# Kernel optimization log

Measured on AMD Instinct MI355X. Metric: run time of the kernel, lower is better.

Reference implementation:

```python
import jax, jax.numpy as jnp
import numpy as np

RESO = 32          # grid_resolution
HID = 32           # hidden_dim
CDIM = 32          # c_dim
NBLK = 5           # n_blocks
PAD = 0.1          # padding
L = 10             # positional encoding frequencies -> dim 60


def setup_inputs() -> dict:
    key = jax.random.key(0)
    ks = jax.random.split(key, 12)
    B, T = 2, 200000
    p = jax.random.uniform(ks[0], (B, T, 3), jnp.float32, -0.5, 0.5)
    s = 0.05
    return {
        "p": p,
        "fc_pos_w": jax.random.normal(ks[1], (60, 2 * HID), jnp.float32) * s,
        "fc_pos_b": jax.random.normal(ks[2], (2 * HID,), jnp.float32) * s,
        "blk_fc0_w": jax.random.normal(ks[3], (NBLK, 2 * HID, HID), jnp.float32) * s,
        "blk_fc0_b": jax.random.normal(ks[4], (NBLK, HID), jnp.float32) * s,
        "blk_fc1_w": jax.random.normal(ks[5], (NBLK, HID, HID), jnp.float32) * s,
        "blk_fc1_b": jax.random.normal(ks[6], (NBLK, HID), jnp.float32) * s,
        "blk_sc_w": jax.random.normal(ks[7], (NBLK, 2 * HID, HID), jnp.float32) * s,  # shortcut, no bias
        "fc_c_w": jax.random.normal(ks[8], (HID, CDIM), jnp.float32) * s,
        "fc_c_b": jax.random.normal(ks[9], (CDIM,), jnp.float32) * s,
    }


def _pos_encode(p):
    # p in [-0.5,0.5] -> [-2,0] after 2p-1 (matches torch impl: p = 2*p - 1)
    q = 2.0 * p - 1.0
    freqs = (jnp.pi * (2.0 ** jnp.arange(L, dtype=jnp.float32)))  # [L]
    a = q[..., None, :] * freqs[:, None]                          # [B,T,L,3]
    pe = jnp.stack([jnp.sin(a), jnp.cos(a)], axis=-2)             # [B,T,L,2,3]
    return pe.reshape(*p.shape[:-1], 2 * L * 3)                   # [B,T,60]


def _normalize_3d(p):
    p_nor = p / (1.0 + PAD + 1e-3) + 0.5
    return jnp.clip(p_nor, 0.0, 1.0 - 1e-3)


def _coord2index(p_nor):
    x = jnp.floor(p_nor * RESO).astype(jnp.int32)                  # [B,T,3]
    return x[..., 0] + RESO * (x[..., 1] + RESO * x[..., 2])       # [B,T]


def _resblock(x, w0, b0, w1, b1, ws):
    h = jax.nn.relu(jax.nn.relu(x) @ w0 + b0)
    return x @ ws + (jax.nn.relu(h) @ w1 + b1)


def reference(p, fc_pos_w, fc_pos_b, blk_fc0_w, blk_fc0_b, blk_fc1_w, blk_fc1_b,
              blk_sc_w, fc_c_w, fc_c_b):
    B, T, _ = p.shape
    G = RESO ** 3
    p_nor = _normalize_3d(p)
    idx = _coord2index(p_nor)                                      # [B,T]
    gidx = (idx + jnp.arange(B, dtype=jnp.int32)[:, None] * G).reshape(-1)  # [B*T]

    net = _pos_encode(p) @ fc_pos_w + fc_pos_b                     # [B,T,64]
    net = _resblock(net, blk_fc0_w[0], blk_fc0_b[0], blk_fc1_w[0], blk_fc1_b[0], blk_sc_w[0])
    for i in range(1, NBLK):
        # pool_local: scatter_max per grid cell, gather back to points
        flat = net.reshape(B * T, HID)
        cell = jax.ops.segment_max(flat, gidx, num_segments=B * G)  # [B*G,HID]
        pooled = cell[gidx].reshape(B, T, HID)
        net = jnp.concatenate([net, pooled], axis=-1)               # [B,T,64]
        net = _resblock(net, blk_fc0_w[i], blk_fc0_b[i], blk_fc1_w[i], blk_fc1_b[i], blk_sc_w[i])

    c = net @ fc_c_w + fc_c_b                                       # [B,T,CDIM]

    # generate_grid_features: scatter_mean into grid (empty cells = 0)
    cf = c.reshape(B * T, CDIM)
    sums = jax.ops.segment_sum(cf, gidx, num_segments=B * G)        # [B*G,CDIM]
    cnt = jax.ops.segment_sum(jnp.ones((B * T, 1), c.dtype), gidx, num_segments=B * G)
    mean = sums / jnp.maximum(cnt, 1.0)
    fea_grid = mean.reshape(B, G, CDIM).transpose(0, 2, 1).reshape(B, CDIM, RESO, RESO, RESO)
    return fea_grid
```

## Files before the change

kernel.cpp:

```cpp
#include <hip/hip_runtime.h>
#include <math.h>

#define TPTS 200000
#define BB 2
#define NPTS (BB*TPTS)
#define GRID3 32768
#define BG 65536
#define SROWS 176

typedef __attribute__((ext_vector_type(8))) __bf16 bf16x8;
typedef __attribute__((ext_vector_type(4))) float f32x4;
typedef unsigned short ushort_t;

#define MFMA16(a,b,c) __builtin_amdgcn_mfma_f32_16x16x32_bf16(a,b,c,0,0,0)

__device__ __forceinline__ void split8(const float* v, bf16x8& hi, bf16x8& lo)
{
#pragma unroll
  for (int j = 0; j < 8; j++) {
    float f = v[j];
    __bf16 h = (__bf16)f;
    hi[j] = h;
    lo[j] = (__bf16)(f - (float)h);
  }
}

__device__ __forceinline__ void relumask8(
    const float* v, const bf16x8& xh, const bf16x8& xl, bf16x8& rh, bf16x8& rl)
{
#pragma unroll
  for (int j = 0; j < 8; j++) {
    bool neg = v[j] < 0.f;
    rh[j] = neg ? (__bf16)0.f : xh[j];
    rl[j] = neg ? (__bf16)0.f : xl[j];
  }
}

__device__ __forceinline__ int cellof(float p0, float p1, float p2, int t)
{
  const float DEN = (float)(1.0 + 0.1 + 1e-3);
  const float HI  = (float)(1.0 - 1e-3);
  float n0 = fminf(fmaxf(p0/DEN + 0.5f, 0.f), HI);
  float n1 = fminf(fmaxf(p1/DEN + 0.5f, 0.f), HI);
  float n2 = fminf(fmaxf(p2/DEN + 0.5f, 0.f), HI);
  int c0 = (int)floorf(n0*32.f), c1 = (int)floorf(n1*32.f), c2 = (int)floorf(n2*32.f);
  return c0 + 32*(c1 + 32*c2) + (t >= TPTS ? GRID3 : 0);
}

__global__ __launch_bounds__(256) void k_hist(
    const float* __restrict__ p, int* __restrict__ gbuf, int* __restrict__ hist)
{
  int t = blockIdx.x*256 + threadIdx.x;
  if (t >= NPTS) return;
  int g = cellof(p[3*t], p[3*t+1], p[3*t+2], t);
  gbuf[t] = g;
  atomicAdd(hist + g, 1);
}

__global__ __launch_bounds__(256) void k_scanA(
    const int* __restrict__ hist, int* __restrict__ texcl, int* __restrict__ bsum)
{
  __shared__ int sm[256];
  int tid = threadIdx.x;
  int t = blockIdx.x*256 + tid;
  int v = hist[t];
  sm[tid] = v; __syncthreads();
  for (int off = 1; off < 256; off <<= 1) {
    int x = sm[tid];
    int u = (tid >= off) ? sm[tid-off] : 0;
    __syncthreads();
    sm[tid] = x + u;
    __syncthreads();
  }
  texcl[t] = sm[tid] - v;
  if (tid == 255) bsum[blockIdx.x] = sm[255];
}

__global__ __launch_bounds__(256) void k_scanB(
    const int* __restrict__ bsum, int* __restrict__ boff)
{
  __shared__ int sm[256];
  int tid = threadIdx.x;
  int v = bsum[tid];
  sm[tid] = v; __syncthreads();
  for (int off = 1; off < 256; off <<= 1) {
    int x = sm[tid];
    int u = (tid >= off) ? sm[tid-off] : 0;
    __syncthreads();
    sm[tid] = x + u;
    __syncthreads();
  }
  boff[tid] = sm[tid] - v;
}

__global__ __launch_bounds__(256) void k_scanC(
    const int* __restrict__ texcl, const int* __restrict__ boff,
    int* __restrict__ start, int* __restrict__ cursor)
{
  int t = blockIdx.x*256 + threadIdx.x;
  int v = boff[blockIdx.x] + texcl[t];
  start[t] = v; cursor[t] = v;
  if (t == 0) start[BG] = NPTS;
}

__global__ __launch_bounds__(256) void k_scatter(
    const float* __restrict__ p, const int* __restrict__ gbuf,
    int* __restrict__ cursor, float* __restrict__ p_sorted, int* __restrict__ gsort)
{
  int t = blockIdx.x*256 + threadIdx.x;
  if (t >= NPTS) return;
  int g = gbuf[t];
  int slot = atomicAdd(cursor + g, 1);
  gsort[slot] = g;
  p_sorted[3*slot]   = p[3*t];
  p_sorted[3*slot+1] = p[3*t+1];
  p_sorted[3*slot+2] = p[3*t+2];
}

__global__ void k_pack(
    const float* __restrict__ f0w, const float* __restrict__ scw,
    const float* __restrict__ f1w, const float* __restrict__ wc,
    const float* __restrict__ Wp,
    ushort_t* __restrict__ wpack)
{
  int f = blockIdx.x, l = threadIdx.x;
  if (f >= 104) {
    int idx = f - 104;
    int c = idx >> 3, t = (idx >> 1) & 3, e = idx & 1;
#pragma unroll
    for (int j = 0; j < 8; j++) {
      int k = c*32 + (l>>4)*8 + j, n = t*16 + (l&15);
      float v = (k < 60) ? Wp[k*64 + n] : 0.f;
      __bf16 h = (__bf16)v;
      __bf16 out = (e == 0) ? h : (__bf16)(v - (float)h);
      union { __bf16 b; ushort_t u; } cv; cv.b = out;
      wpack[((size_t)f*64 + l)*8 + j] = cv.u;
    }
    return;
  }
  const float* W; int c, t, e;
  if (f < 100) {
    int s = f / 20, r = f % 20;
    if (r < 8)       { W = f0w + s*2048; c = r>>2;        t = (r>>1)&1; e = r&1; }
    else if (r < 16) { int q = r-8;  W = scw + s*2048; c = q>>2; t = (q>>1)&1; e = q&1; }
    else             { int q = r-16; W = f1w + s*1024; c = 0;    t = q>>1;     e = q&1; }
  } else { int q = f-100; W = wc; c = 0; t = q>>1; e = q&1; }
#pragma unroll
  for (int j = 0; j < 8; j++) {
    int k = c*32 + (l>>4)*8 + j, n = t*16 + (l&15);
    float v = W[k*32 + n];
    __bf16 h = (__bf16)v;
    __bf16 out = (e == 0) ? h : (__bf16)(v - (float)h);
    union { __bf16 b; ushort_t u; } cv; cv.b = out;
    wpack[((size_t)f*64 + l)*8 + j] = cv.u;
  }
}

__global__ __launch_bounds__(256) void k_fused0(
    const float* __restrict__ ps,
    const ushort_t* __restrict__ wpPE, const float* __restrict__ bp,
    const ushort_t* __restrict__ wp,
    const float* __restrict__ b0, const float* __restrict__ b1,
    float* __restrict__ net)
{
  __shared__ float xlds[4][16*68];
  __shared__ float hbuf[4][16*36];
  int wave = threadIdx.x >> 6, lane = threadIdx.x & 63;
  int m = lane & 15, q = lane >> 4;
  int pbase = (blockIdx.x*4 + wave)*16;
  int pt = pbase + m;

  float p0 = ps[3*pt], p1 = ps[3*pt+1], p2 = ps[3*pt+2];
  float u0 = 2.f*p0 - 1.f, u1 = 2.f*p1 - 1.f, u2 = 2.f*p2 - 1.f;
  const float PIF = 3.14159265358979323846f;

  float pe[2][8];
#pragma unroll
  for (int c2 = 0; c2 < 2; c2++) {
#pragma unroll
    for (int jj = 0; jj < 8; jj++) {
      int e = c2*32 + q*8 + jj;
      int l = (e * 43691) >> 18;
      int r = e - l*6;
      bool issin = (r < 3);
      int d = issin ? r : (r - 3);
      float ud = (d == 0) ? u0 : ((d == 1) ? u1 : u2);
      float xval = ldexpf(ud, l);
      float red = xval - 2.f*rintf(0.5f*xval);
      float ang = PIF*red + (issin ? 0.f : 1.5707963267948966f);
      float v = __sinf(ang);
      pe[c2][jj] = (e < 60) ? v : 0.f;
    }
  }
  bf16x8 peh[2], pel[2];
  split8(pe[0], peh[0], pel[0]);
  split8(pe[1], peh[1], pel[1]);

  f32x4 xacc[4];
#pragma unroll
  for (int t = 0; t < 4; t++) {
    float bb = bp[t*16 + m];
    xacc[t] = (f32x4){bb,bb,bb,bb};
  }
#pragma unroll
  for (int c2 = 0; c2 < 2; c2++)
#pragma unroll
    for (int t = 0; t < 4; t++) {
      bf16x8 bh = *(const bf16x8*)(wpPE + ((size_t)((c2*4+t)*2    )*64 + lane)*8);
      bf16x8 bl = *(const bf16x8*)(wpPE + ((size_t)((c2*4+t)*2 + 1)*64 + lane)*8);
      xacc[t] = MFMA16(peh[c2], bh, xacc[t]);
      xacc[t] = MFMA16(pel[c2], bh, xacc[t]);
      xacc[t] = MFMA16(peh[c2], bl, xacc[t]);
    }

  float* xl = xlds[wave];
#pragma unroll
  for (int t = 0; t < 4; t++)
#pragma unroll
    for (int r = 0; r < 4; r++)
      xl[(q*4+r)*68 + t*16 + m] = xacc[t][r];
  __syncthreads();

  float xv[2][8];
#pragma unroll
  for (int c2 = 0; c2 < 2; c2++)
#pragma unroll
    for (int jj = 0; jj < 8; jj++)
      xv[c2][jj] = xl[m*68 + c2*32 + q*8 + jj];

  bf16x8 w0f[2][2][2], wsf[2][2][2], w1f[2][2];
#pragma unroll
  for (int c = 0; c < 2; c++)
#pragma unroll
    for (int t = 0; t < 2; t++)
#pragma unroll
      for (int e = 0; e < 2; e++) {
        w0f[c][t][e] = *(const bf16x8*)(wp + ((size_t)(((c*2+t)*2+e)    )*64 + lane)*8);
        wsf[c][t][e] = *(const bf16x8*)(wp + ((size_t)(((c*2+t)*2+e) + 8)*64 + lane)*8);
      }
#pragma unroll
  for (int t = 0; t < 2; t++)
#pragma unroll
    for (int e = 0; e < 2; e++)
      w1f[t][e] = *(const bf16x8*)(wp + ((size_t)(16 + t*2 + e)*64 + lane)*8);

  bf16x8 axh[2], axl[2], arh[2], arl[2];
#pragma unroll
  for (int c = 0; c < 2; c++) {
    split8(xv[c], axh[c], axl[c]);
    relumask8(xv[c], axh[c], axl[c], arh[c], arl[c]);
  }

  f32x4 hacc[2], yacc[2];
#pragma unroll
  for (int t = 0; t < 2; t++) {
    float bb0 = b0[m + 16*t], bb1 = b1[m + 16*t];
    hacc[t] = (f32x4){bb0,bb0,bb0,bb0};
    yacc[t] = (f32x4){bb1,bb1,bb1,bb1};
  }

#pragma unroll
  for (int c = 0; c < 2; c++)
#pragma unroll
    for (int t = 0; t < 2; t++) {
      hacc[t] = MFMA16(arh[c], w0f[c][t][0], hacc[t]);
      hacc[t] = MFMA16(arl[c], w0f[c][t][0], hacc[t]);
      hacc[t] = MFMA16(arh[c], w0f[c][t][1], hacc[t]);
      yacc[t] = MFMA16(axh[c], wsf[c][t][0], yacc[t]);
      yacc[t] = MFMA16(axl[c], wsf[c][t][0], yacc[t]);
      yacc[t] = MFMA16(axh[c], wsf[c][t][1], yacc[t]);
    }

  float* hb = hbuf[wave];
#pragma unroll
  for (int t = 0; t < 2; t++)
#pragma unroll
    for (int r = 0; r < 4; r++)
      hb[(q*4+r)*36 + m + 16*t] = fmaxf(hacc[t][r], 0.f);
  __syncthreads();
  float hv[8];
#pragma unroll
  for (int j = 0; j < 8; j++) hv[j] = hb[m*36 + q*8 + j];
  bf16x8 hh, hl; split8(hv, hh, hl);
#pragma unroll
  for (int t = 0; t < 2; t++) {
    yacc[t] = MFMA16(hh, w1f[t][0], yacc[t]);
    yacc[t] = MFMA16(hl, w1f[t][0], yacc[t]);
    yacc[t] = MFMA16(hh, w1f[t][1], yacc[t]);
  }

#pragma unroll
  for (int t = 0; t < 2; t++)
#pragma unroll
    for (int r = 0; r < 4; r++)
      net[(size_t)(pbase + q*4 + r)*32 + m + 16*t] = yacc[t][r];
}

__global__ __launch_bounds__(256) void k_stage_f(
    const float* __restrict__ netin, float* __restrict__ netout,
    const int* __restrict__ gsort, const int* __restrict__ start,
    const ushort_t* __restrict__ wp,
    const float* __restrict__ b0, const float* __restrict__ b1)
{
  __shared__ float sbuf[SROWS*36];
  int tid = threadIdx.x;
  int P0 = blockIdx.x*64;
  int s = start[gsort[P0]];
  int e = start[gsort[P0+63] + 1];
  int n = e - s; if (n > SROWS) n = SROWS;

  for (int idx = tid; idx < n*8; idx += 256) {
    int r = idx >> 3, c = idx & 7;
    *(f32x4*)(sbuf + r*36 + c*4) =
      *(const f32x4*)(netin + ((size_t)(s + r))*32 + c*4);
  }
  __syncthreads();

  int wave = tid >> 6, lane = tid & 63;
  int m = lane & 15, q = lane >> 4;
  int pbase = P0 + wave*16;
  int pt = pbase + m;
  int g = gsort[pt];
  int cs = start[g] - s, ce = start[g+1] - s;

  float xv[2][8];
  {
    const float* xr = sbuf + (pt - s)*36 + q*8;
    *(f32x4*)&xv[0][0] = *(const f32x4*)xr;
    *(f32x4*)&xv[0][4] = *(const f32x4*)(xr + 4);
  }
  {
    f32x4 ma = (f32x4){-INFINITY,-INFINITY,-INFINITY,-INFINITY};
    f32x4 mb = ma;
    for (int k = cs; k < ce; k++) {
      const float* rr = sbuf + k*36 + q*8;
      f32x4 va = *(const f32x4*)rr;
      f32x4 vb = *(const f32x4*)(rr + 4);
      ma.x = fmaxf(ma.x, va.x); ma.y = fmaxf(ma.y, va.y);
      ma.z = fmaxf(ma.z, va.z); ma.w = fmaxf(ma.w, va.w);
      mb.x = fmaxf(mb.x, vb.x); mb.y = fmaxf(mb.y, vb.y);
      mb.z = fmaxf(mb.z, vb.z); mb.w = fmaxf(mb.w, vb.w);
    }
    *(f32x4*)&xv[1][0] = ma;
    *(f32x4*)&xv[1][4] = mb;
  }

  bf16x8 w0f[2][2][2], wsf[2][2][2], w1f[2][2];
#pragma unroll
  for (int c = 0; c < 2; c++)
#pragma unroll
    for (int t = 0; t < 2; t++)
#pragma unroll
      for (int e2 = 0; e2 < 2; e2++) {
        w0f[c][t][e2] = *(const bf16x8*)(wp + ((size_t)(((c*2+t)*2+e2)    )*64 + lane)*8);
        wsf[c][t][e2] = *(const bf16x8*)(wp + ((size_t)(((c*2+t)*2+e2) + 8)*64 + lane)*8);
      }
#pragma unroll
  for (int t = 0; t < 2; t++)
#pragma unroll
    for (int e2 = 0; e2 < 2; e2++)
      w1f[t][e2] = *(const bf16x8*)(wp + ((size_t)(16 + t*2 + e2)*64 + lane)*8);

  bf16x8 axh[2], axl[2], arh[2], arl[2];
#pragma unroll
  for (int c = 0; c < 2; c++) {
    split8(xv[c], axh[c], axl[c]);
    relumask8(xv[c], axh[c], axl[c], arh[c], arl[c]);
  }

  f32x4 hacc[2], yacc[2];
#pragma unroll
  for (int t = 0; t < 2; t++) {
    float bb0 = b0[m + 16*t], bb1 = b1[m + 16*t];
    hacc[t] = (f32x4){bb0,bb0,bb0,bb0};
    yacc[t] = (f32x4){bb1,bb1,bb1,bb1};
  }

#pragma unroll
  for (int c = 0; c < 2; c++)
#pragma unroll
    for (int t = 0; t < 2; t++) {
      hacc[t] = MFMA16(arh[c], w0f[c][t][0], hacc[t]);
      hacc[t] = MFMA16(arl[c], w0f[c][t][0], hacc[t]);
      hacc[t] = MFMA16(arh[c], w0f[c][t][1], hacc[t]);
      yacc[t] = MFMA16(axh[c], wsf[c][t][0], yacc[t]);
      yacc[t] = MFMA16(axl[c], wsf[c][t][0], yacc[t]);
      yacc[t] = MFMA16(axh[c], wsf[c][t][1], yacc[t]);
    }

  __syncthreads();
  float* hb = sbuf + wave*576;
#pragma unroll
  for (int t = 0; t < 2; t++)
#pragma unroll
    for (int r = 0; r < 4; r++)
      hb[(q*4+r)*36 + m + 16*t] = fmaxf(hacc[t][r], 0.f);
  __syncthreads();
  float hv[8];
#pragma unroll
  for (int j = 0; j < 8; j++) hv[j] = hb[m*36 + q*8 + j];
  bf16x8 hh, hl; split8(hv, hh, hl);
#pragma unroll
  for (int t = 0; t < 2; t++) {
    yacc[t] = MFMA16(hh, w1f[t][0], yacc[t]);
    yacc[t] = MFMA16(hl, w1f[t][0], yacc[t]);
    yacc[t] = MFMA16(hh, w1f[t][1], yacc[t]);
  }

#pragma unroll
  for (int t = 0; t < 2; t++)
#pragma unroll
    for (int r = 0; r < 4; r++)
      netout[(size_t)(pbase + q*4 + r)*32 + m + 16*t] = yacc[t][r];
}

__global__ __launch_bounds__(256) void k_final_f(
    const float* __restrict__ netin, float* __restrict__ netout,
    const int* __restrict__ gsort, const int* __restrict__ start,
    const ushort_t* __restrict__ wp, const ushort_t* __restrict__ wpc,
    const float* __restrict__ b0, const float* __restrict__ b1,
    const float* __restrict__ bc)
{
  __shared__ float sbuf[SROWS*36];
  int tid = threadIdx.x;
  int P0 = blockIdx.x*64;
  int s = start[gsort[P0]];
  int e = start[gsort[P0+63] + 1];
  int n = e - s; if (n > SROWS) n = SROWS;

  for (int idx = tid; idx < n*8; idx += 256) {
    int r = idx >> 3, c = idx & 7;
    *(f32x4*)(sbuf + r*36 + c*4) =
      *(const f32x4*)(netin + ((size_t)(s + r))*32 + c*4);
  }
  __syncthreads();

  int wave = tid >> 6, lane = tid & 63;
  int m = lane & 15, q = lane >> 4;
  int pbase = P0 + wave*16;
  int pt = pbase + m;
  int g = gsort[pt];
  int cs = start[g] - s, ce = start[g+1] - s;

  float xv[2][8];
  {
    const float* xr = sbuf + (pt - s)*36 + q*8;
    *(f32x4*)&xv[0][0] = *(const f32x4*)xr;
    *(f32x4*)&xv[0][4] = *(const f32x4*)(xr + 4);
  }
  {
    f32x4 ma = (f32x4){-INFINITY,-INFINITY,-INFINITY,-INFINITY};
    f32x4 mb = ma;
    for (int k = cs; k < ce; k++) {
      const float* rr = sbuf + k*36 + q*8;
      f32x4 va = *(const f32x4*)rr;
      f32x4 vb = *(const f32x4*)(rr + 4);
      ma.x = fmaxf(ma.x, va.x); ma.y = fmaxf(ma.y, va.y);
      ma.z = fmaxf(ma.z, va.z); ma.w = fmaxf(ma.w, va.w);
      mb.x = fmaxf(mb.x, vb.x); mb.y = fmaxf(mb.y, vb.y);
      mb.z = fmaxf(mb.z, vb.z); mb.w = fmaxf(mb.w, vb.w);
    }
    *(f32x4*)&xv[1][0] = ma;
    *(f32x4*)&xv[1][4] = mb;
  }

  bf16x8 w0f[2][2][2], wsf[2][2][2], w1f[2][2], wcf[2][2];
#pragma unroll
  for (int c = 0; c < 2; c++)
#pragma unroll
    for (int t = 0; t < 2; t++)
#pragma unroll
      for (int e2 = 0; e2 < 2; e2++) {
        w0f[c][t][e2] = *(const bf16x8*)(wp + ((size_t)(((c*2+t)*2+e2)    )*64 + lane)*8);
        wsf[c][t][e2] = *(const bf16x8*)(wp + ((size_t)(((c*2+t)*2+e2) + 8)*64 + lane)*8);
      }
#pragma unroll
  for (int t = 0; t < 2; t++)
#pragma unroll
    for (int e2 = 0; e2 < 2; e2++) {
      w1f[t][e2] = *(const bf16x8*)(wp  + ((size_t)(16 + t*2 + e2)*64 + lane)*8);
      wcf[t][e2] = *(const bf16x8*)(wpc + ((size_t)(     t*2 + e2)*64 + lane)*8);
    }

  bf16x8 axh[2], axl[2], arh[2], arl[2];
#pragma unroll
  for (int c = 0; c < 2; c++) {
    split8(xv[c], axh[c], axl[c]);
    relumask8(xv[c], axh[c], axl[c], arh[c], arl[c]);
  }

  f32x4 hacc[2], yacc[2];
#pragma unroll
  for (int t = 0; t < 2; t++) {
    float bb0 = b0[m + 16*t], bb1 = b1[m + 16*t];
    hacc[t] = (f32x4){bb0,bb0,bb0,bb0};
    yacc[t] = (f32x4){bb1,bb1,bb1,bb1};
  }

#pragma unroll
  for (int c = 0; c < 2; c++)
#pragma unroll
    for (int t = 0; t < 2; t++) {
      hacc[t] = MFMA16(arh[c], w0f[c][t][0], hacc[t]);
      hacc[t] = MFMA16(arl[c], w0f[c][t][0], hacc[t]);
      hacc[t] = MFMA16(arh[c], w0f[c][t][1], hacc[t]);
      yacc[t] = MFMA16(axh[c], wsf[c][t][0], yacc[t]);
      yacc[t] = MFMA16(axl[c], wsf[c][t][0], yacc[t]);
      yacc[t] = MFMA16(axh[c], wsf[c][t][1], yacc[t]);
    }

  __syncthreads();
  float* hb = sbuf + wave*576;
  float* yb = sbuf + 4*576 + wave*576;
#pragma unroll
  for (int t = 0; t < 2; t++)
#pragma unroll
    for (int r = 0; r < 4; r++)
      hb[(q*4+r)*36 + m + 16*t] = fmaxf(hacc[t][r], 0.f);
  __syncthreads();
  float hv[8];
#pragma unroll
  for (int j = 0; j < 8; j++) hv[j] = hb[m*36 + q*8 + j];
  bf16x8 hh, hl; split8(hv, hh, hl);
#pragma unroll
  for (int t = 0; t < 2; t++) {
    yacc[t] = MFMA16(hh, w1f[t][0], yacc[t]);
    yacc[t] = MFMA16(hl, w1f[t][0], yacc[t]);
    yacc[t] = MFMA16(hh, w1f[t][1], yacc[t]);
  }

#pragma unroll
  for (int t = 0; t < 2; t++)
#pragma unroll
    for (int r = 0; r < 4; r++)
      yb[(q*4+r)*36 + m + 16*t] = yacc[t][r];
  __syncthreads();
  float yv[8];
#pragma unroll
  for (int j = 0; j < 8; j++) yv[j] = yb[m*36 + q*8 + j];
  bf16x8 yh, yl; split8(yv, yh, yl);

  f32x4 cacc[2];
#pragma unroll
  for (int t = 0; t < 2; t++) {
    float bb = bc[m + 16*t];
    cacc[t] = (f32x4){bb,bb,bb,bb};
    cacc[t] = MFMA16(yh, wcf[t][0], cacc[t]);
    cacc[t] = MFMA16(yl, wcf[t][0], cacc[t]);
    cacc[t] = MFMA16(yh, wcf[t][1], cacc[t]);
  }

#pragma unroll
  for (int t = 0; t < 2; t++)
#pragma unroll
    for (int r = 0; r < 4; r++)
      netout[(size_t)(pbase + q*4 + r)*32 + m + 16*t] = cacc[t][r];
}

__global__ __launch_bounds__(256) void k_mean(
    const float* __restrict__ net, const int* __restrict__ start,
    float* __restrict__ outp)
{
  int tid = blockIdx.x*256 + threadIdx.x;
  int c = tid >> 3, sub = tid & 7;
  int s = start[c], e = start[c+1];
  f32x4 sum = (f32x4){0.f,0.f,0.f,0.f};
  for (int k = s; k < e; k++) {
    f32x4 v = *(const f32x4*)(net + (size_t)k*32 + sub*4);
    sum.x += v.x; sum.y += v.y; sum.z += v.z; sum.w += v.w;
  }
  float inv = (e > s) ? 1.f/(float)(e - s) : 0.f;
  int b = c >> 15, cell = c & 32767;
  size_t ob = ((size_t)b << 20) + cell;
#pragma unroll
  for (int jj = 0; jj < 4; jj++) {
    int ch = sub*4 + jj;
    float v = ((const float*)&sum)[jj] * inv;
    outp[ob + ((size_t)ch << 15)] = v;
  }
}

extern "C" void kernel_launch(void* const* d_in, const int* in_sizes, int n_in,
                              void* d_out, int out_size, void* d_ws, size_t ws_size,
                              hipStream_t stream)
{
  const float* p   = (const float*)d_in[0];
  const float* Wp  = (const float*)d_in[1];
  const float* bp  = (const float*)d_in[2];
  const float* f0w = (const float*)d_in[3];
  const float* f0b = (const float*)d_in[4];
  const float* f1w = (const float*)d_in[5];
  const float* f1b = (const float*)d_in[6];
  const float* scw = (const float*)d_in[7];
  const float* wc  = (const float*)d_in[8];
  const float* bc  = (const float*)d_in[9];
  float* outp = (float*)d_out;

  char* wsb = (char*)d_ws;
  float*    netA     = (float*)wsb;
  float*    netB     = netA + (size_t)NPTS*32;
  int*      gbuf     = (int*)(netB + (size_t)NPTS*32);
  int*      gsort    = gbuf + NPTS;
  int*      hist     = gsort + NPTS;
  int*      start    = hist + BG;
  int*      cursor   = start + BG + 1;
  int*      texcl    = cursor + BG;
  int*      bsum     = texcl + BG;
  int*      boff     = bsum + 256;
  ushort_t* wpack    = (ushort_t*)(boff + 256);
  float*    p_sorted = (float*)(wpack + (size_t)120*512);

  dim3 blk(256);
  dim3 gpts((NPTS + 255)/256);
  dim3 gmfma(NPTS/64);
  dim3 gcell((BG*8)/256);
  dim3 gscan(BG/256);

  hipMemsetAsync(hist, 0, (size_t)BG*4, stream);
  hipLaunchKernelGGL(k_hist, gpts, blk, 0, stream, p, gbuf, hist);
  hipLaunchKernelGGL(k_scanA, gscan, blk, 0, stream, hist, texcl, bsum);
  hipLaunchKernelGGL(k_scanB, dim3(1), blk, 0, stream, bsum, boff);
  hipLaunchKernelGGL(k_scanC, gscan, blk, 0, stream, texcl, boff, start, cursor);
  hipLaunchKernelGGL(k_scatter, gpts, blk, 0, stream, p, gbuf, cursor, p_sorted, gsort);
  hipLaunchKernelGGL(k_pack, dim3(120), dim3(64), 0, stream, f0w, scw, f1w, wc, Wp, wpack);
  hipLaunchKernelGGL(k_fused0, gmfma, blk, 0, stream,
                     p_sorted, wpack + (size_t)104*512, bp,
                     wpack + (size_t)0*20*512, f0b + 0*32, f1b + 0*32, netA);
  hipLaunchKernelGGL(k_stage_f, gmfma, blk, 0, stream, netA, netB, gsort, start,
                     wpack + (size_t)1*20*512, f0b + 1*32, f1b + 1*32);
  hipLaunchKernelGGL(k_stage_f, gmfma, blk, 0, stream, netB, netA, gsort, start,
                     wpack + (size_t)2*20*512, f0b + 2*32, f1b + 2*32);
  hipLaunchKernelGGL(k_stage_f, gmfma, blk, 0, stream, netA, netB, gsort, start,
                     wpack + (size_t)3*20*512, f0b + 3*32, f1b + 3*32);
  hipLaunchKernelGGL(k_final_f, gmfma, blk, 0, stream, netB, netA, gsort, start,
                     wpack + (size_t)4*20*512, wpack + (size_t)100*512,
                     f0b + 4*32, f1b + 4*32, bc);
  hipLaunchKernelGGL(k_mean, gcell, blk, 0, stream, netA, start, outp);
}
```

Baseline: 333.9 us.

## Drop LDS staging of cell rows and use wave-local fences instead of block barriers

The stage kernels no longer copy each block's contiguous range of sorted rows into shared memory. Each lane now reads its own row and its cell's neighbour rows for the max pool straight from global memory, relying on cache. Block-wide __syncthreads between per-wave LDS transposes become __threadfence_block, since each wave only touches its own LDS slice, and the LDS buffers are shrunk and reused. This cuts shared-memory footprint and barrier stalls, which should raise occupancy, at the cost of repeated uncoalesced global reads during the pooling loop. It also relies on fences being enough for intra-wave ordering of LDS.

```diff
diff --git a/kernel.cpp b/kernel.cpp
--- a/kernel.cpp
+++ b/kernel.cpp
@@ -6,7 +6,6 @@
 #define NPTS (BB*TPTS)
 #define GRID3 32768
 #define BG 65536
-#define SROWS 176
 
 typedef __attribute__((ext_vector_type(8))) __bf16 bf16x8;
 typedef __attribute__((ext_vector_type(4))) float f32x4;
@@ -164,7 +163,6 @@
     float* __restrict__ net)
 {
   __shared__ float xlds[4][16*68];
-  __shared__ float hbuf[4][16*36];
   int wave = threadIdx.x >> 6, lane = threadIdx.x & 63;
   int m = lane & 15, q = lane >> 4;
   int pbase = (blockIdx.x*4 + wave)*16;
@@ -219,7 +217,7 @@
 #pragma unroll
     for (int r = 0; r < 4; r++)
       xl[(q*4+r)*68 + t*16 + m] = xacc[t][r];
-  __syncthreads();
+  __threadfence_block();
 
   float xv[2][8];
 #pragma unroll
@@ -227,6 +225,7 @@
 #pragma unroll
     for (int jj = 0; jj < 8; jj++)
       xv[c2][jj] = xl[m*68 + c2*32 + q*8 + jj];
+  __threadfence_block();
 
   bf16x8 w0f[2][2][2], wsf[2][2][2], w1f[2][2];
 #pragma unroll
@@ -271,13 +270,13 @@
       yacc[t] = MFMA16(axh[c], wsf[c][t][1], yacc[t]);
     }
 
-  float* hb = hbuf[wave];
+  float* hb = xl;
 #pragma unroll
   for (int t = 0; t < 2; t++)
 #pragma unroll
     for (int r = 0; r < 4; r++)
       hb[(q*4+r)*36 + m + 16*t] = fmaxf(hacc[t][r], 0.f);
-  __syncthreads();
+  __threadfence_block();
   float hv[8];
 #pragma unroll
   for (int j = 0; j < 8; j++) hv[j] = hb[m*36 + q*8 + j];
@@ -302,30 +301,18 @@
     const ushort_t* __restrict__ wp,
     const float* __restrict__ b0, const float* __restrict__ b1)
 {
-  __shared__ float sbuf[SROWS*36];
+  __shared__ float hbuf[4][576];
   int tid = threadIdx.x;
-  int P0 = blockIdx.x*64;
-  int s = start[gsort[P0]];
-  int e = start[gsort[P0+63] + 1];
-  int n = e - s; if (n > SROWS) n = SROWS;
-
-  for (int idx = tid; idx < n*8; idx += 256) {
-    int r = idx >> 3, c = idx & 7;
-    *(f32x4*)(sbuf + r*36 + c*4) =
-      *(const f32x4*)(netin + ((size_t)(s + r))*32 + c*4);
-  }
-  __syncthreads();
-
   int wave = tid >> 6, lane = tid & 63;
   int m = lane & 15, q = lane >> 4;
-  int pbase = P0 + wave*16;
+  int pbase = blockIdx.x*64 + wave*16;
   int pt = pbase + m;
   int g = gsort[pt];
-  int cs = start[g] - s, ce = start[g+1] - s;
+  int cs = start[g], ce = start[g+1];
 
   float xv[2][8];
   {
-    const float* xr = sbuf + (pt - s)*36 + q*8;
+    const float* xr = netin + (size_t)pt*32 + q*8;
     *(f32x4*)&xv[0][0] = *(const f32x4*)xr;
     *(f32x4*)&xv[0][4] = *(const f32x4*)(xr + 4);
   }
@@ -333,7 +320,7 @@
     f32x4 ma = (f32x4){-INFINITY,-INFINITY,-INFINITY,-INFINITY};
     f32x4 mb = ma;
     for (int k = cs; k < ce; k++) {
-      const float* rr = sbuf + k*36 + q*8;
+      const float* rr = netin + (size_t)k*32 + q*8;
       f32x4 va = *(const f32x4*)rr;
       f32x4 vb = *(const f32x4*)(rr + 4);
       ma.x = fmaxf(ma.x, va.x); ma.y = fmaxf(ma.y, va.y);
@@ -388,14 +375,13 @@
       yacc[t] = MFMA16(axh[c], wsf[c][t][1], yacc[t]);
     }
 
-  __syncthreads();
-  float* hb = sbuf + wave*576;
+  float* hb = hbuf[wave];
 #pragma unroll
   for (int t = 0; t < 2; t++)
 #pragma unroll
     for (int r = 0; r < 4; r++)
       hb[(q*4+r)*36 + m + 16*t] = fmaxf(hacc[t][r], 0.f);
-  __syncthreads();
+  __threadfence_block();
   float hv[8];
 #pragma unroll
   for (int j = 0; j < 8; j++) hv[j] = hb[m*36 + q*8 + j];
@@ -421,30 +407,18 @@
     const float* __restrict__ b0, const float* __restrict__ b1,
     const float* __restrict__ bc)
 {
-  __shared__ float sbuf[SROWS*36];
+  __shared__ float hbuf[4][576];
   int tid = threadIdx.x;
-  int P0 = blockIdx.x*64;
-  int s = start[gsort[P0]];
-  int e = start[gsort[P0+63] + 1];
-  int n = e - s; if (n > SROWS) n = SROWS;
-
-  for (int idx = tid; idx < n*8; idx += 256) {
-    int r = idx >> 3, c = idx & 7;
-    *(f32x4*)(sbuf + r*36 + c*4) =
-      *(const f32x4*)(netin + ((size_t)(s + r))*32 + c*4);
-  }
-  __syncthreads();
-
   int wave = tid >> 6, lane = tid & 63;
   int m = lane & 15, q = lane >> 4;
-  int pbase = P0 + wave*16;
+  int pbase = blockIdx.x*64 + wave*16;
   int pt = pbase + m;
   int g = gsort[pt];
-  int cs = start[g] - s, ce = start[g+1] - s;
+  int cs = start[g], ce = start[g+1];
 
   float xv[2][8];
   {
-    const float* xr = sbuf + (pt - s)*36 + q*8;
+    const float* xr = netin + (size_t)pt*32 + q*8;
     *(f32x4*)&xv[0][0] = *(const f32x4*)xr;
     *(f32x4*)&xv[0][4] = *(const f32x4*)(xr + 4);
   }
@@ -452,7 +426,7 @@
     f32x4 ma = (f32x4){-INFINITY,-INFINITY,-INFINITY,-INFINITY};
     f32x4 mb = ma;
     for (int k = cs; k < ce; k++) {
-      const float* rr = sbuf + k*36 + q*8;
+      const float* rr = netin + (size_t)k*32 + q*8;
       f32x4 va = *(const f32x4*)rr;
       f32x4 vb = *(const f32x4*)(rr + 4);
       ma.x = fmaxf(ma.x, va.x); ma.y = fmaxf(ma.y, va.y);
@@ -509,19 +483,18 @@
       yacc[t] = MFMA16(axh[c], wsf[c][t][1], yacc[t]);
     }
 
-  __syncthreads();
-  float* hb = sbuf + wave*576;
-  float* yb = sbuf + 4*576 + wave*576;
+  float* hb = hbuf[wave];
 #pragma unroll
   for (int t = 0; t < 2; t++)
 #pragma unroll
     for (int r = 0; r < 4; r++)
       hb[(q*4+r)*36 + m + 16*t] = fmaxf(hacc[t][r], 0.f);
-  __syncthreads();
+  __threadfence_block();
   float hv[8];
 #pragma unroll
   for (int j = 0; j < 8; j++) hv[j] = hb[m*36 + q*8 + j];
   bf16x8 hh, hl; split8(hv, hh, hl);
+  __threadfence_block();
 #pragma unroll
   for (int t = 0; t < 2; t++) {
     yacc[t] = MFMA16(hh, w1f[t][0], yacc[t]);
@@ -533,11 +506,11 @@
   for (int t = 0; t < 2; t++)
 #pragma unroll
     for (int r = 0; r < 4; r++)
-      yb[(q*4+r)*36 + m + 16*t] = yacc[t][r];
-  __syncthreads();
+      hb[(q*4+r)*36 + m + 16*t] = yacc[t][r];
+  __threadfence_block();
   float yv[8];
 #pragma unroll
-  for (int j = 0; j < 8; j++) yv[j] = yb[m*36 + q*8 + j];
+  for (int j = 0; j < 8; j++) yv[j] = hb[m*36 + q*8 + j];
   bf16x8 yh, yl; split8(yv, yh, yl);
 
   f32x4 cacc[2];
```

Result: slower. 376.2 us (+12.7%).
